# Kernel optimization log

Hardware: AMD Instinct MI355X
Metric: run time of the kernel (lower is better)

## Reference

```python
import jax, jax.numpy as jnp
import numpy as np

OUT_FEATURES = 4096
IN_FEATURES = 4096
R = 16
DIST = 4
N_FREQ = 10000
SCALING = 150.0


def setup_inputs() -> dict:
    key = jax.random.key(0)
    k_x, k_w, k_b, k_s, k_a, k_i = jax.random.split(key, 6)
    x = jax.random.normal(k_x, (4, 2048, IN_FEATURES), dtype=jnp.float32)
    base_w = jax.random.normal(k_w, (OUT_FEATURES, IN_FEATURES), dtype=jnp.float32) * 0.02
    base_b = jax.random.normal(k_b, (OUT_FEATURES,), dtype=jnp.float32) * 0.02
    spectrum = jax.random.normal(k_s, (N_FREQ,), dtype=jnp.float32)
    hora_A = jax.random.normal(k_a, (R, IN_FEATURES), dtype=jnp.float32)
    # torch uses randperm(r*out_features)[:n_frequency] -> unique flat indices
    idx = jax.random.permutation(k_i, R * OUT_FEATURES)[:N_FREQ].astype(jnp.int32)
    return {"x": x, "base_w": base_w, "base_b": base_b,
            "spectrum": spectrum, "hora_A": hora_A, "idx": idx}


def reference(x, base_w, base_b, spectrum, hora_A, idx):
    # --- get_delta_weight ---
    rows = idx // R            # index into out_features
    cols = idx % R             # index into r
    dense_spectrum = jnp.zeros((OUT_FEATURES, R), dtype=spectrum.dtype)
    dense_spectrum = dense_spectrum.at[rows, cols].set(spectrum)
    # chunk_size = ceil(out/dist) = 1024; out divisible by dist -> pure reshape
    chunks = dense_spectrum.reshape(DIST, OUT_FEATURES // DIST, R)
    B = jnp.fft.ifft2(chunks, axes=(-2, -1)).real.astype(spectrum.dtype)
    B = B.reshape(OUT_FEATURES, R)
    delta_w = (B * SCALING) @ hora_A          # [out_features, in_features]
    # --- forward: base linear + adapter linear ---
    base_out = jnp.einsum('bsi,oi->bso', x, base_w) + base_b
    result = base_out + jnp.einsum('bsi,oi->bso', x, delta_w)
    return result
```

## Files before the change

kernel.cpp:

```cpp
#include <hip/hip_runtime.h>
#include <hip/hip_bf16.h>


#define OUTF 4096
#define INF  4096
#define NFREQ 10000
#define MDIM 8192
#define KT   (INF / 64)

typedef __attribute__((ext_vector_type(8))) short bf16x8;
typedef __attribute__((ext_vector_type(4))) float f32x4;

__device__ __forceinline__ unsigned int bf16pack2(float a, float b) {
    unsigned int ua = __builtin_bit_cast(unsigned int, a);
    unsigned int ub = __builtin_bit_cast(unsigned int, b);
    ua = (ua + 0x7fffu + ((ua >> 16) & 1u)) >> 16;
    ub = (ub + 0x7fffu + ((ub >> 16) & 1u)) & 0xffff0000u;
    return ua | ub;
}

__device__ __forceinline__ void async_copy16(const void* g, void* l) {
    __builtin_amdgcn_global_load_lds(
        (__attribute__((address_space(1))) void*)(g),
        (__attribute__((address_space(3))) void*)(l),
        16, 0, 0);
}

__global__ __launch_bounds__(256) void build_B_kernel(
        const float* __restrict__ spectrum, const int* __restrict__ idx,
        float* __restrict__ Bout) {
    __shared__ int   s_jk[6144];
    __shared__ float s_v[6144];
    __shared__ int   s_cnt;
    const int tid = threadIdx.x;
    if (tid == 0) s_cnt = 0;
    __syncthreads();
    const int p = blockIdx.x >> 6;
    for (int i = tid; i < NFREQ; i += 256) {
        int id = idx[i];
        if ((id >> 14) == p) {
            int pos = atomicAdd(&s_cnt, 1);
            if (pos < 6144) {
                s_jk[pos] = id & 16383;
                s_v[pos]  = spectrum[i];
            }
        }
    }
    __syncthreads();
    const int cnt = (s_cnt < 6144) ? s_cnt : 6144;
    const int gid = blockIdx.x * 256 + tid;
    const int o = gid >> 4;
    const int r = gid & 15;
    const int m = o & 1023;
    const float c = 6.283185307179586f / 16384.f;
    float acc = 0.f;
    for (int t = 0; t < cnt; ++t) {
        int jk = s_jk[t];
        int j = jk >> 4, k = jk & 15;
        int ph = (((j * m) & 1023) << 4) + (((k * r) & 15) << 10);
        ph &= 16383;
        acc += s_v[t] * __cosf((float)ph * c);
    }
    Bout[gid] = acc * (150.f / 16384.f);
}

__global__ __launch_bounds__(256) void build_w_kernel(
        const float* __restrict__ bw, const float* __restrict__ A,
        const float* __restrict__ Bs, unsigned short* __restrict__ W) {
    const int n0 = blockIdx.x * 8;
    __shared__ float sB[8][16];
    if (threadIdx.x < 128)
        ((float*)sB)[threadIdx.x] = Bs[n0 * 16 + threadIdx.x];
    __syncthreads();
    const float4* A4 = (const float4*)A;
    const float4* bw4 = (const float4*)bw;
    uint2* W2 = (uint2*)W;
#pragma unroll 1
    for (int q = 0; q < 4; ++q) {
        const int c4 = threadIdx.x + q * 256;
        float4 a[16];
#pragma unroll
        for (int r = 0; r < 16; ++r) a[r] = A4[r * 1024 + c4];
#pragma unroll 1
        for (int nn = 0; nn < 8; ++nn) {
            const int n = n0 + nn;
            float4 wv = bw4[n * 1024 + c4];
#pragma unroll
            for (int r = 0; r < 16; ++r) {
                float s = sB[nn][r];
                wv.x += s * a[r].x; wv.y += s * a[r].y;
                wv.z += s * a[r].z; wv.w += s * a[r].w;
            }
            W2[n * 1024 + c4] = make_uint2(bf16pack2(wv.x, wv.y),
                                           bf16pack2(wv.z, wv.w));
        }
    }
}

__global__ __launch_bounds__(256) void cvt_x_kernel(
        const float4* __restrict__ x, uint2* __restrict__ xb, int n4) {
    for (int i = blockIdx.x * blockDim.x + threadIdx.x; i < n4;
         i += gridDim.x * blockDim.x) {
        float4 v = x[i];
        xb[i] = make_uint2(bf16pack2(v.x, v.y), bf16pack2(v.z, v.w));
    }
}

__global__ __launch_bounds__(512, 2) void gemm256_kernel(
        const unsigned short* __restrict__ Xb,
        const unsigned short* __restrict__ Wb,
        const float* __restrict__ bias, float* __restrict__ C) {
    __shared__ __align__(1024) char lds[131072];

    const int tid  = threadIdx.x;
    const int lane = tid & 63;
    const int wid  = tid >> 6;
    const int wm   = wid >> 2;
    const int wn   = wid & 3;

    int bid = blockIdx.x;
    bid = (bid & 7) * 64 + (bid >> 3);
    const int tm = bid >> 4;
    const int tn = bid & 15;
    const int arow0 = tm * 256;
    const int brow0 = tn * 256;

    const int srow  = tid >> 3;
    const int scole = (((tid & 7) * 16) ^ ((srow & 7) << 4)) >> 1;
    const int sldsb = tid * 16;

    const int l15 = lane & 15;
    const int kx0 = ((lane >> 4) * 16) ^ ((lane & 7) << 4);
    const int kx1 = kx0 ^ 64;
    const int abase0 = (wm * 128 + l15) * 128;
    const int bbase0 = 32768 + (wn * 64 + l15) * 128;

    f32x4 acc[8][4] = {};
    bf16x8 af[4][2], bfa[2][2], bfb[2][2];

#define STAGE_HALF(mat, grow0, t, ldsbase) do {                               \
        const unsigned short* _s =                                            \
            (mat) + ((grow0) + srow) * INF + (t) * 64 + scole;                \
        async_copy16(_s, lds + (ldsbase) + sldsb);                            \
        async_copy16(_s + 64 * INF, lds + (ldsbase) + 8192 + sldsb);          \
    } while (0)

#define LDA(DB, m, kh) (*(const bf16x8*)(lds + (DB) + abase0 + (m) * 2048 + ((kh) ? kx1 : kx0)))
#define LDB(DB, n, kh) (*(const bf16x8*)(lds + (DB) + bbase0 + (n) * 2048 + ((kh) ? kx1 : kx0)))

#define MFMA(a, b, c) __builtin_amdgcn_mfma_f32_16x16x32_bf16((a), (b), (c), 0, 0, 0)

#define PH_OPEN()  __builtin_amdgcn_s_barrier();                              \
                   asm volatile("s_waitcnt lgkmcnt(0)" ::: "memory");         \
                   __builtin_amdgcn_s_setprio(1)
#define PH_CLOSE() __builtin_amdgcn_s_setprio(0);                             \
                   __builtin_amdgcn_s_barrier();                              \
                   asm volatile("" ::: "memory")

#define ITER(CUR, OTH, t) do {                                                \
                     \
    _Pragma("unroll") for (int m = 0; m < 4; ++m) {                           \
        af[m][0] = LDA(CUR, m, 0); af[m][1] = LDA(CUR, m, 1); }               \
    _Pragma("unroll") for (int n = 0; n < 2; ++n) {                           \
        bfa[n][0] = LDB(CUR, n, 0); bfa[n][1] = LDB(CUR, n, 1); }             \
    if ((t) + 1 < KT) STAGE_HALF(Xb, arow0 + 128, (t) + 1, (OTH) + 16384);    \
    PH_OPEN();                                                                \
    _Pragma("unroll") for (int m = 0; m < 4; ++m)                             \
        _Pragma("unroll") for (int n = 0; n < 2; ++n) {                       \
            acc[m][n] = MFMA(af[m][0], bfa[n][0], acc[m][n]);                 \
            acc[m][n] = MFMA(af[m][1], bfa[n][1], acc[m][n]); }               \
    PH_CLOSE();                                                               \
                     \
    _Pragma("unroll") for (int n = 0; n < 2; ++n) {                           \
        bfb[n][0] = LDB(CUR, n + 2, 0); bfb[n][1] = LDB(CUR, n + 2, 1); }     \
    if ((t) + 1 < KT) STAGE_HALF(Wb, brow0, (t) + 1, (OTH) + 32768);          \
    PH_OPEN();                                                                \
    _Pragma("unroll") for (int m = 0; m < 4; ++m)                             \
        _Pragma("unroll") for (int n = 0; n < 2; ++n) {                       \
            acc[m][n + 2] = MFMA(af[m][0], bfb[n][0], acc[m][n + 2]);         \
            acc[m][n + 2] = MFMA(af[m][1], bfb[n][1], acc[m][n + 2]); }       \
    PH_CLOSE();                                                               \
                     \
    _Pragma("unroll") for (int m = 0; m < 4; ++m) {                           \
        af[m][0] = LDA(CUR, m + 4, 0); af[m][1] = LDA(CUR, m + 4, 1); }       \
    if ((t) + 1 < KT) STAGE_HALF(Wb, brow0 + 128, (t) + 1, (OTH) + 49152);    \
    PH_OPEN();                                                                \
    _Pragma("unroll") for (int m = 0; m < 4; ++m)                             \
        _Pragma("unroll") for (int n = 0; n < 2; ++n) {                       \
            acc[m + 4][n] = MFMA(af[m][0], bfa[n][0], acc[m + 4][n]);         \
            acc[m + 4][n] = MFMA(af[m][1], bfa[n][1], acc[m + 4][n]); }       \
    PH_CLOSE();                                                               \
      \
    if ((t) + 2 < KT) STAGE_HALF(Xb, arow0, (t) + 2, (CUR));                  \
    __builtin_amdgcn_s_barrier();                                             \
    asm volatile("s_waitcnt lgkmcnt(0)" ::: "memory");                        \
    __builtin_amdgcn_s_setprio(1);                                            \
    _Pragma("unroll") for (int m = 0; m < 4; ++m)                             \
        _Pragma("unroll") for (int n = 0; n < 2; ++n) {                       \
            acc[m + 4][n + 2] = MFMA(af[m][0], bfb[n][0], acc[m + 4][n + 2]); \
            acc[m + 4][n + 2] = MFMA(af[m][1], bfb[n][1], acc[m + 4][n + 2]); \
        }                                                                     \
    __builtin_amdgcn_s_setprio(0);                                            \
    if ((t) + 2 < KT) { asm volatile("s_waitcnt vmcnt(2)" ::: "memory"); }    \
    else              { asm volatile("s_waitcnt vmcnt(0)" ::: "memory"); }    \
    __builtin_amdgcn_s_barrier();                                             \
    asm volatile("" ::: "memory");                                            \
} while (0)

    STAGE_HALF(Xb, arow0,       0, 0);
    STAGE_HALF(Xb, arow0 + 128, 0, 16384);
    STAGE_HALF(Wb, brow0,       0, 32768);
    STAGE_HALF(Wb, brow0 + 128, 0, 49152);
    STAGE_HALF(Xb, arow0,       1, 65536);
    asm volatile("s_waitcnt vmcnt(2)" ::: "memory");
    __builtin_amdgcn_s_barrier();
    asm volatile("" ::: "memory");

    for (int t = 0; t < KT; t += 2) {
        ITER(0, 65536, t);
        ITER(65536, 0, t + 1);
    }

#pragma unroll
    for (int n = 0; n < 4; ++n) {
        const int gcol = brow0 + wn * 64 + n * 16 + l15;
        const float bv = bias[gcol];
#pragma unroll
        for (int m = 0; m < 8; ++m) {
            const int grow = arow0 + wm * 128 + m * 16 + (lane >> 4) * 4;
#pragma unroll
            for (int rg = 0; rg < 4; ++rg)
                C[(grow + rg) * OUTF + gcol] = acc[m][n][rg] + bv;
        }
    }
#undef STAGE_HALF
#undef LDA
#undef LDB
#undef MFMA
#undef PH_OPEN
#undef PH_CLOSE
#undef ITER
}

extern "C" void kernel_launch(void* const* d_in, const int* in_sizes, int n_in,
                              void* d_out, int out_size, void* d_ws, size_t ws_size,
                              hipStream_t stream) {
    const float* x    = (const float*)d_in[0];
    const float* bw   = (const float*)d_in[1];
    const float* bb   = (const float*)d_in[2];
    const float* spec = (const float*)d_in[3];
    const float* ha   = (const float*)d_in[4];
    const int*   idx  = (const int*)d_in[5];
    float* out = (float*)d_out;

    char* ws = (char*)d_ws;
    float*          Bbuf = (float*)ws;
    unsigned short* Wb   = (unsigned short*)(ws + 262144);
    unsigned short* Xb   = (unsigned short*)(ws + 262144 + 33554432);

    build_B_kernel<<<256, 256, 0, stream>>>(spec, idx, Bbuf);
    build_w_kernel<<<512, 256, 0, stream>>>(bw, ha, Bbuf, Wb);
    cvt_x_kernel<<<2048, 256, 0, stream>>>((const float4*)x, (uint2*)Xb,
                                           (MDIM * INF) / 4);
    gemm256_kernel<<<512, 512, 0, stream>>>(Xb, Wb, bb, out);
}
```

Before: 404.1 us.

## Rebalance GEMM prefetch schedule and split build_B work across more blocks

The build_B kernel now launches four times as many blocks. Each block compacts its matching frequencies with a wave ballot instead of shared atomics, splits the cosine sum over four thread quarters and reduces them through shared memory. The GEMM main loop is reordered so the next tile's X halves are staged early and W halves are prefetched two tiles ahead, with finer vmcnt waits and the B fragments for the next tile preloaded. This aims to raise parallelism in the small prologue kernel and hide more global-load latency in the GEMM, at the cost of more complex wait counts and an entry cap lowered from 6144 to 3072.

After: 495.3 us. 1.23x slower.

```diff
diff --git a/kernel.cpp b/kernel.cpp
--- a/kernel.cpp
+++ b/kernel.cpp
@@ -29,39 +29,56 @@
 __global__ __launch_bounds__(256) void build_B_kernel(
         const float* __restrict__ spectrum, const int* __restrict__ idx,
         float* __restrict__ Bout) {
-    __shared__ int   s_jk[6144];
-    __shared__ float s_v[6144];
+    __shared__ int2  s_jkv[3072];
+    __shared__ float s_part[4][64];
     __shared__ int   s_cnt;
-    const int tid = threadIdx.x;
-    if (tid == 0) s_cnt = 0;
+    const int tid  = threadIdx.x;
+    const int gid0 = blockIdx.x * 64;
+    const int p    = gid0 >> 14;
+
+    if (tid < 64) {
+        int base = 0;
+        for (int i0 = 0; i0 < NFREQ; i0 += 64) {
+            const int i = i0 + tid;
+            bool m = false; int id = 0;
+            if (i < NFREQ) { id = idx[i]; m = ((id >> 14) == p); }
+            unsigned long long bal = __ballot(m);
+            if (m) {
+                int pos = base + __popcll(bal & ((1ull << tid) - 1ull));
+                if (pos < 3072)
+                    s_jkv[pos] = make_int2(id & 16383,
+                                           __builtin_bit_cast(int, spectrum[i]));
+            }
+            base += __popcll(bal);
+        }
+        if (tid == 0) s_cnt = (base < 3072) ? base : 3072;
+    }
     __syncthreads();
-    const int p = blockIdx.x >> 6;
-    for (int i = tid; i < NFREQ; i += 256) {
-        int id = idx[i];
-        if ((id >> 14) == p) {
-            int pos = atomicAdd(&s_cnt, 1);
-            if (pos < 6144) {
-                s_jk[pos] = id & 16383;
-                s_v[pos]  = spectrum[i];
-            }
-        }
-    }
-    __syncthreads();
-    const int cnt = (s_cnt < 6144) ? s_cnt : 6144;
-    const int gid = blockIdx.x * 256 + tid;
-    const int o = gid >> 4;
-    const int r = gid & 15;
-    const int m = o & 1023;
-    const float c = 6.283185307179586f / 16384.f;
+    const int cnt  = s_cnt;
+    const int qtr  = tid >> 6;
+    const int ol   = tid & 63;
+    const int gid  = gid0 + ol;
+    const int o    = gid >> 4;
+    const int r    = gid & 15;
+    const int m    = o & 1023;
+    const int qlen = (cnt + 3) >> 2;
+    const int t0   = qtr * qlen;
+    const int t1   = (t0 + qlen < cnt) ? t0 + qlen : cnt;
+    const float c  = 6.283185307179586f / 16384.f;
     float acc = 0.f;
-    for (int t = 0; t < cnt; ++t) {
-        int jk = s_jk[t];
-        int j = jk >> 4, k = jk & 15;
+    for (int t = t0; t < t1; ++t) {
+        const int2 jv = s_jkv[t];
+        const int j = jv.x >> 4, k = jv.x & 15;
         int ph = (((j * m) & 1023) << 4) + (((k * r) & 15) << 10);
         ph &= 16383;
-        acc += s_v[t] * __cosf((float)ph * c);
-    }
-    Bout[gid] = acc * (150.f / 16384.f);
+        acc += __builtin_bit_cast(float, jv.y) * __cosf((float)ph * c);
+    }
+    s_part[qtr][ol] = acc;
+    __syncthreads();
+    if (tid < 64) {
+        float s = s_part[0][tid] + s_part[1][tid] + s_part[2][tid] + s_part[3][tid];
+        Bout[gid0 + tid] = s * (150.f / 16384.f);
+    }
 }
 
 __global__ __launch_bounds__(256) void build_w_kernel(
@@ -147,53 +164,66 @@
 
 #define LDA(DB, m, kh) (*(const bf16x8*)(lds + (DB) + abase0 + (m) * 2048 + ((kh) ? kx1 : kx0)))
 #define LDB(DB, n, kh) (*(const bf16x8*)(lds + (DB) + bbase0 + (n) * 2048 + ((kh) ? kx1 : kx0)))
-
 #define MFMA(a, b, c) __builtin_amdgcn_mfma_f32_16x16x32_bf16((a), (b), (c), 0, 0, 0)
-
-#define PH_OPEN()  __builtin_amdgcn_s_barrier();                              \
-                   asm volatile("s_waitcnt lgkmcnt(0)" ::: "memory");         \
-                   __builtin_amdgcn_s_setprio(1)
-#define PH_CLOSE() __builtin_amdgcn_s_setprio(0);                             \
-                   __builtin_amdgcn_s_barrier();                              \
-                   asm volatile("" ::: "memory")
-
-#define ITER(CUR, OTH, t) do {                                                \
-                     \
+#define BARRIER() do { asm volatile("" ::: "memory");                         \
+                       __builtin_amdgcn_s_barrier();                          \
+                       asm volatile("" ::: "memory"); } while (0)
+
+#define TILE(CUR, OTH, s) do {                                                \
+     \
     _Pragma("unroll") for (int m = 0; m < 4; ++m) {                           \
         af[m][0] = LDA(CUR, m, 0); af[m][1] = LDA(CUR, m, 1); }               \
-    _Pragma("unroll") for (int n = 0; n < 2; ++n) {                           \
-        bfa[n][0] = LDB(CUR, n, 0); bfa[n][1] = LDB(CUR, n, 1); }             \
-    if ((t) + 1 < KT) STAGE_HALF(Xb, arow0 + 128, (t) + 1, (OTH) + 16384);    \
-    PH_OPEN();                                                                \
+    if ((s) + 1 < KT) STAGE_HALF(Xb, arow0, (s) + 1, (OTH) + 0);              \
+    asm volatile("s_waitcnt vmcnt(6)" ::: "memory");                          \
+    BARRIER();                                                                \
+    asm volatile("s_waitcnt lgkmcnt(0)" ::: "memory");                        \
+    __builtin_amdgcn_s_setprio(1);                                            \
     _Pragma("unroll") for (int m = 0; m < 4; ++m)                             \
         _Pragma("unroll") for (int n = 0; n < 2; ++n) {                       \
             acc[m][n] = MFMA(af[m][0], bfa[n][0], acc[m][n]);                 \
             acc[m][n] = MFMA(af[m][1], bfa[n][1], acc[m][n]); }               \
-    PH_CLOSE();                                                               \
-                     \
+    __builtin_amdgcn_s_setprio(0);                                            \
+    BARRIER();                                                                \
+        \
     _Pragma("unroll") for (int n = 0; n < 2; ++n) {                           \
         bfb[n][0] = LDB(CUR, n + 2, 0); bfb[n][1] = LDB(CUR, n + 2, 1); }     \
-    if ((t) + 1 < KT) STAGE_HALF(Wb, brow0, (t) + 1, (OTH) + 32768);          \
-    PH_OPEN();                                                                \
+    if ((s) + 1 < KT) STAGE_HALF(Xb, arow0 + 128, (s) + 1, (OTH) + 16384);    \
+    asm volatile("s_waitcnt vmcnt(6)" ::: "memory");                          \
+    BARRIER();                                                                \
+    asm volatile("s_waitcnt lgkmcnt(0)" ::: "memory");                        \
+    __builtin_amdgcn_s_setprio(1);                                            \
     _Pragma("unroll") for (int m = 0; m < 4; ++m)                             \
         _Pragma("unroll") for (int n = 0; n < 2; ++n) {                       \
             acc[m][n + 2] = MFMA(af[m][0], bfb[n][0], acc[m][n + 2]);         \
             acc[m][n + 2] = MFMA(af[m][1], bfb[n][1], acc[m][n + 2]); }       \
-    PH_CLOSE();                                                               \
-                     \
+    __builtin_amdgcn_s_setprio(0);                                            \
+    BARRIER();                                                                \
+     \
     _Pragma("unroll") for (int m = 0; m < 4; ++m) {                           \
         af[m][0] = LDA(CUR, m + 4, 0); af[m][1] = LDA(CUR, m + 4, 1); }       \
-    if ((t) + 1 < KT) STAGE_HALF(Wb, brow0 + 128, (t) + 1, (OTH) + 49152);    \
-    PH_OPEN();                                                                \
+    if ((s) + 2 < KT) STAGE_HALF(Wb, brow0, (s) + 2, (CUR) + 32768);          \
+    if ((s) < KT - 2) { asm volatile("s_waitcnt vmcnt(6)" ::: "memory"); }    \
+    else              { asm volatile("s_waitcnt vmcnt(4)" ::: "memory"); }    \
+    BARRIER();                                                                \
+    asm volatile("s_waitcnt lgkmcnt(0)" ::: "memory");                        \
+    __builtin_amdgcn_s_setprio(1);                                            \
     _Pragma("unroll") for (int m = 0; m < 4; ++m)                             \
         _Pragma("unroll") for (int n = 0; n < 2; ++n) {                       \
             acc[m + 4][n] = MFMA(af[m][0], bfa[n][0], acc[m + 4][n]);         \
             acc[m + 4][n] = MFMA(af[m][1], bfa[n][1], acc[m + 4][n]); }       \
-    PH_CLOSE();                                                               \
-      \
-    if ((t) + 2 < KT) STAGE_HALF(Xb, arow0, (t) + 2, (CUR));                  \
-    __builtin_amdgcn_s_barrier();                                             \
-    asm volatile("s_waitcnt lgkmcnt(0)" ::: "memory");                        \
+    __builtin_amdgcn_s_setprio(0);                                            \
+    BARRIER();                                                                \
+       \
+       \
+    if ((s) + 1 < KT) {                                                       \
+        _Pragma("unroll") for (int n = 0; n < 2; ++n) {                       \
+            bfa[n][0] = LDB(OTH, n, 0); bfa[n][1] = LDB(OTH, n, 1); }         \
+    }                                                                         \
+    if ((s) + 2 < KT) STAGE_HALF(Wb, brow0 + 128, (s) + 2, (CUR) + 49152);    \
+    if ((s) < KT - 2) { asm volatile("s_waitcnt vmcnt(4)" ::: "memory"); }    \
+    else              { asm volatile("s_waitcnt vmcnt(0)" ::: "memory"); }    \
+    BARRIER();                                                                \
+    asm volatile("s_waitcnt lgkmcnt(4)" ::: "memory");                        \
     __builtin_amdgcn_s_setprio(1);                                            \
     _Pragma("unroll") for (int m = 0; m < 4; ++m)                             \
         _Pragma("unroll") for (int n = 0; n < 2; ++n) {                       \
@@ -201,24 +231,25 @@
             acc[m + 4][n + 2] = MFMA(af[m][1], bfb[n][1], acc[m + 4][n + 2]); \
         }                                                                     \
     __builtin_amdgcn_s_setprio(0);                                            \
-    if ((t) + 2 < KT) { asm volatile("s_waitcnt vmcnt(2)" ::: "memory"); }    \
-    else              { asm volatile("s_waitcnt vmcnt(0)" ::: "memory"); }    \
-    __builtin_amdgcn_s_barrier();                                             \
-    asm volatile("" ::: "memory");                                            \
+    BARRIER();                                                                \
 } while (0)
 
     STAGE_HALF(Xb, arow0,       0, 0);
     STAGE_HALF(Xb, arow0 + 128, 0, 16384);
     STAGE_HALF(Wb, brow0,       0, 32768);
     STAGE_HALF(Wb, brow0 + 128, 0, 49152);
-    STAGE_HALF(Xb, arow0,       1, 65536);
-    asm volatile("s_waitcnt vmcnt(2)" ::: "memory");
-    __builtin_amdgcn_s_barrier();
-    asm volatile("" ::: "memory");
-
-    for (int t = 0; t < KT; t += 2) {
-        ITER(0, 65536, t);
-        ITER(65536, 0, t + 1);
+    STAGE_HALF(Wb, brow0,       1, 65536 + 32768);
+    STAGE_HALF(Wb, brow0 + 128, 1, 65536 + 49152);
+    asm volatile("s_waitcnt vmcnt(4)" ::: "memory");
+    BARRIER();
+#pragma unroll
+    for (int n = 0; n < 2; ++n) {
+        bfa[n][0] = LDB(0, n, 0); bfa[n][1] = LDB(0, n, 1);
+    }
+
+    for (int s = 0; s < KT; s += 2) {
+        TILE(0, 65536, s);
+        TILE(65536, 0, s + 1);
     }
 
 #pragma unroll
@@ -237,9 +268,8 @@
 #undef LDA
 #undef LDB
 #undef MFMA
-#undef PH_OPEN
-#undef PH_CLOSE
-#undef ITER
+#undef BARRIER
+#undef TILE
 }
 
 extern "C" void kernel_launch(void* const* d_in, const int* in_sizes, int n_in,
@@ -258,7 +288,7 @@
     unsigned short* Wb   = (unsigned short*)(ws + 262144);
     unsigned short* Xb   = (unsigned short*)(ws + 262144 + 33554432);
 
-    build_B_kernel<<<256, 256, 0, stream>>>(spec, idx, Bbuf);
+    build_B_kernel<<<1024, 256, 0, stream>>>(spec, idx, Bbuf);
     build_w_kernel<<<512, 256, 0, stream>>>(bw, ha, Bbuf, Wb);
     cvt_x_kernel<<<2048, 256, 0, stream>>>((const float4*)x, (uint2*)Xb,
                                            (MDIM * INF) / 4);
```
